# Performance work log

Measured on AMD Instinct MI355X. Metric: run time of the kernel, lower is better.

The kernel has to match this reference:

```python
import jax, jax.numpy as jnp
import numpy as np

N_NODES = 50000
N_EDGES = 800000


def gcn_layer(x, edge_index, W, b):
    # GCNConv with normalize=False: out[i] = sum_{(j->i) in E} (x_j @ W) + b
    src, dst = edge_index[0], edge_index[1]
    h = x @ W                          # [N, F_out] transform first (cheaper)
    msg = h[src]                       # [E, F_out] gather
    agg = jax.ops.segment_sum(msg, dst, num_segments=x.shape[0])  # scatter-sum
    return agg + b


def setup_inputs() -> dict:
    key = jax.random.key(0)
    ks = jax.random.split(key, 6)
    x = jax.random.normal(ks[0], (N_NODES, 128), dtype=jnp.float32)
    edge_index = jax.random.randint(ks[1], (2, N_EDGES), 0, N_NODES, dtype=jnp.int64)
    # Glorot-ish scaling for stability through 3 layers
    W1 = jax.random.normal(ks[2], (128, 256), dtype=jnp.float32) * (1.0 / np.sqrt(128))
    W2 = jax.random.normal(ks[3], (256, 256), dtype=jnp.float32) * (1.0 / np.sqrt(256))
    W3 = jax.random.normal(ks[4], (256, 256), dtype=jnp.float32) * (1.0 / np.sqrt(256))
    b1 = jnp.zeros((256,), jnp.float32)
    b2 = jnp.zeros((256,), jnp.float32)
    b3 = jnp.zeros((256,), jnp.float32)
    return {"x": x, "edge_index": edge_index, "W1": W1, "b1": b1,
            "W2": W2, "b2": b2, "W3": W3, "b3": b3}


def reference(x, edge_index, W1, b1, W2, b2, W3, b3):
    h = jax.nn.relu(gcn_layer(x, edge_index, W1, b1))
    h = jax.nn.relu(gcn_layer(h, edge_index, W2, b2))
    h = jax.nn.relu(gcn_layer(h, edge_index, W3, b3))
    return h
```

## Files before the change

kernel.cpp:

```cpp
#include <hip/hip_runtime.h>
#include <hip/hip_bf16.h>


#define NBIN 98
#define BINSH 9
#define CAP 10240

typedef short bf16x8 __attribute__((ext_vector_type(8)));
typedef float f32x4 __attribute__((ext_vector_type(4)));
typedef unsigned u32x4 __attribute__((ext_vector_type(4)));

__device__ __forceinline__ short f2bf(float f) {
    __hip_bfloat16 b = __float2bfloat16(f);
    return *reinterpret_cast<short*>(&b);
}

__device__ __forceinline__ void acc8(float* a, u32x4 v) {
#pragma unroll
    for (int i = 0; i < 4; ++i) {
        union { unsigned u; float f; } lo, hi;
        lo.u = v[i] << 16;
        hi.u = v[i] & 0xFFFF0000u;
        a[2 * i]     += lo.f;
        a[2 * i + 1] += hi.f;
    }
}

__global__ void prep(const float* __restrict__ W1, const float* __restrict__ W2,
                     const float* __restrict__ W3, const float4* __restrict__ x,
                     short* __restrict__ Wt1, short* __restrict__ Wt2,
                     short* __restrict__ Wt3, short* __restrict__ xb,
                     int* __restrict__ gcursor, int* __restrict__ off,
                     int E, int N) {
    int idx = blockIdx.x * 256 + threadIdx.x;
    if (idx < 32768) {
        int n = idx >> 7, k = idx & 127;
        Wt1[idx] = f2bf(W1[k * 256 + n]);
    } else if (idx < 98304) {
        int i = idx - 32768, n = i >> 8, k = i & 255;
        Wt2[i] = f2bf(W2[k * 256 + n]);
    } else if (idx < 163840) {
        int i = idx - 98304, n = i >> 8, k = i & 255;
        Wt3[i] = f2bf(W3[k * 256 + n]);
    } else {
        int i = idx - 163840;
        if (i < 1600000) {
            float4 v = x[i];
            short tmp[4] = { f2bf(v.x), f2bf(v.y), f2bf(v.z), f2bf(v.w) };
            *reinterpret_cast<uint2*>(&xb[i * 4]) = *reinterpret_cast<uint2*>(tmp);
        } else {
            int z = i - 1600000;
            if (z < NBIN) gcursor[z] = 0;
            if (z == NBIN) off[N] = E;
        }
    }
}


__launch_bounds__(256)
__global__ void bin_fill(const int* __restrict__ ei, int* __restrict__ gcursor,
                         unsigned* __restrict__ staging, int E) {
    __shared__ int h[NBIN];
    __shared__ int lstart[NBIN];
    __shared__ int gbase[NBIN];
    __shared__ int cur[NBIN];
    __shared__ int scan[256];
    __shared__ unsigned sorted[4096];
    const int t = threadIdx.x;
    for (int i = t; i < NBIN; i += 256) h[i] = 0;
    __syncthreads();
    const int base = blockIdx.x * 4096;
    unsigned w[16];
    int bin[16];
#pragma unroll
    for (int i = 0; i < 16; ++i) {
        int e = base + i * 256 + t;
        if (e < E) {
            int s = ei[e], d = ei[E + e];
            w[i] = ((unsigned)d << 16) | (unsigned)s;
            bin[i] = d >> BINSH;
            atomicAdd(&h[bin[i]], 1);
        } else bin[i] = -1;
    }
    __syncthreads();
    int v = (t < NBIN) ? h[t] : 0;
    scan[t] = v;
    __syncthreads();
    for (int d = 1; d < 256; d <<= 1) {
        int a = (t >= d) ? scan[t - d] : 0;
        __syncthreads();
        scan[t] += a;
        __syncthreads();
    }
    if (t < NBIN) {
        int ex = scan[t] - v;
        lstart[t] = ex;
        cur[t] = ex;
        gbase[t] = v ? atomicAdd(&gcursor[t], v) : 0;
    }
    __syncthreads();
#pragma unroll
    for (int i = 0; i < 16; ++i)
        if (bin[i] >= 0) sorted[atomicAdd(&cur[bin[i]], 1)] = w[i];
    __syncthreads();
    const int nvalid = min(4096, E - base);
    for (int i = t; i < nvalid; i += 256) {
        unsigned u = sorted[i];
        int b = (u >> 16) >> BINSH;
        staging[(size_t)b * CAP + gbase[b] + (i - lstart[b])] = u;
    }
}

__launch_bounds__(256)
__global__ void bin_finalize(const unsigned* __restrict__ staging,
                             const int* __restrict__ cnt,
                             int* __restrict__ off, int* __restrict__ csr, int N) {
    __shared__ int red[256];
    __shared__ int nd_c[512];
    __shared__ int nd_pos[512];
    __shared__ int psum[256];
    const int b = blockIdx.x, t = threadIdx.x;
    const int n = cnt[b];
    const unsigned* reg = staging + (size_t)b * CAP;

    red[t] = (t < b) ? cnt[t] : 0;
    nd_c[t] = 0; nd_c[t + 256] = 0;
    __syncthreads();
    for (int d = 128; d > 0; d >>= 1) {
        if (t < d) red[t] += red[t + d];
        __syncthreads();
    }
    const int gbase = red[0];

    for (int p = t; p < n; p += 256)
        atomicAdd(&nd_c[(reg[p] >> 16) & 511u], 1);
    __syncthreads();
    int c0 = nd_c[2 * t], c1 = nd_c[2 * t + 1];
    psum[t] = c0 + c1;
    __syncthreads();
    for (int d = 1; d < 256; d <<= 1) {
        int a = (t >= d) ? psum[t - d] : 0;
        __syncthreads();
        psum[t] += a;
        __syncthreads();
    }
    int ebase = gbase + (t ? psum[t - 1] : 0);
    int nb0 = b << BINSH;
    nd_pos[2 * t]     = ebase;
    nd_pos[2 * t + 1] = ebase + c0;
    if (nb0 + 2 * t < N)     off[nb0 + 2 * t]     = ebase;
    if (nb0 + 2 * t + 1 < N) off[nb0 + 2 * t + 1] = ebase + c0;
    __syncthreads();
    for (int p = t; p < n; p += 256) {
        unsigned v = reg[p];
        int pos = atomicAdd(&nd_pos[(v >> 16) & 511u], 1);
        csr[pos] = (int)(v & 0xFFFFu);
    }
}


__global__ void gather256(const short* __restrict__ h, short* __restrict__ agg,
                          const int* __restrict__ off, const int* __restrict__ csr,
                          int N) {
    const int gw = (blockIdx.x * blockDim.x + threadIdx.x) >> 6;
    if (gw >= N) return;
    const int lane = threadIdx.x & 63;
    const int half = lane >> 5, l = lane & 31;
    const int col = l * 8;
    const int base = off[gw];
    const int d = off[gw + 1] - base;

    float acc[8];
#pragma unroll
    for (int q = 0; q < 8; ++q) acc[q] = 0.0f;

    int j = 0;
    for (; j + 8 <= d; j += 8) {
        int s0 = csr[base + j + half];
        int s1 = csr[base + j + 2 + half];
        int s2 = csr[base + j + 4 + half];
        int s3 = csr[base + j + 6 + half];
        u32x4 v0 = *reinterpret_cast<const u32x4*>(h + (size_t)s0 * 256 + col);
        u32x4 v1 = *reinterpret_cast<const u32x4*>(h + (size_t)s1 * 256 + col);
        u32x4 v2 = *reinterpret_cast<const u32x4*>(h + (size_t)s2 * 256 + col);
        u32x4 v3 = *reinterpret_cast<const u32x4*>(h + (size_t)s3 * 256 + col);
        acc8(acc, v0); acc8(acc, v1); acc8(acc, v2); acc8(acc, v3);
    }
    for (; j + 2 <= d; j += 2) {
        int s = csr[base + j + half];
        u32x4 v = *reinterpret_cast<const u32x4*>(h + (size_t)s * 256 + col);
        acc8(acc, v);
    }
    if (j < d && half == 0) {
        int s = csr[base + j];
        u32x4 v = *reinterpret_cast<const u32x4*>(h + (size_t)s * 256 + col);
        acc8(acc, v);
    }
#pragma unroll
    for (int q = 0; q < 8; ++q) acc[q] += __shfl_xor(acc[q], 32);
    if (half == 0) {
        short o[8];
#pragma unroll
        for (int q = 0; q < 8; ++q) o[q] = f2bf(acc[q]);
        __builtin_nontemporal_store(*reinterpret_cast<u32x4*>(o),
            reinterpret_cast<u32x4*>(agg + (size_t)gw * 256 + col));
    }
}

__global__ void gather128(const short* __restrict__ h, short* __restrict__ agg,
                          const int* __restrict__ off, const int* __restrict__ csr,
                          int N) {
    const int gw = (blockIdx.x * blockDim.x + threadIdx.x) >> 6;
    if (gw >= N) return;
    const int lane = threadIdx.x & 63;
    const int q4 = lane >> 4, l = lane & 15;
    const int col = l * 8;
    const int base = off[gw];
    const int d = off[gw + 1] - base;

    float acc[8];
#pragma unroll
    for (int q = 0; q < 8; ++q) acc[q] = 0.0f;

    int j = 0;
    for (; j + 8 <= d; j += 8) {
        int s0 = csr[base + j + q4];
        int s1 = csr[base + j + 4 + q4];
        u32x4 v0 = *reinterpret_cast<const u32x4*>(h + (size_t)s0 * 128 + col);
        u32x4 v1 = *reinterpret_cast<const u32x4*>(h + (size_t)s1 * 128 + col);
        acc8(acc, v0); acc8(acc, v1);
    }
    for (; j + 4 <= d; j += 4) {
        int s = csr[base + j + q4];
        u32x4 v = *reinterpret_cast<const u32x4*>(h + (size_t)s * 128 + col);
        acc8(acc, v);
    }
    int rem = d - j;
    if (q4 < rem) {
        int s = csr[base + j + q4];
        u32x4 v = *reinterpret_cast<const u32x4*>(h + (size_t)s * 128 + col);
        acc8(acc, v);
    }
#pragma unroll
    for (int q = 0; q < 8; ++q) {
        acc[q] += __shfl_xor(acc[q], 32);
        acc[q] += __shfl_xor(acc[q], 16);
    }
    if (q4 == 0) {
        short o[8];
#pragma unroll
        for (int q = 0; q < 8; ++q) o[q] = f2bf(acc[q]);
        __builtin_nontemporal_store(*reinterpret_cast<u32x4*>(o),
            reinterpret_cast<u32x4*>(agg + (size_t)gw * 128 + col));
    }
}


template <typename OutT>
__launch_bounds__(512)
__global__ void gemm_bias_relu(const short* __restrict__ A, const short* __restrict__ Wt,
                               const float* __restrict__ bias, OutT* __restrict__ out,
                               int M, int K) {
    __shared__ short As[128][72];
    __shared__ short Bs[256][72];

    const int tid = threadIdx.x;
    const int lane = tid & 63, wid = tid >> 6;
    const int wr = wid >> 2, wc = wid & 3;
    const int lr = lane & 15, lg = lane >> 4;
    const int m0 = blockIdx.x * 128;

    f32x4 acc[4][4];
#pragma unroll
    for (int i = 0; i < 4; ++i)
#pragma unroll
        for (int j = 0; j < 4; ++j)
#pragma unroll
            for (int r = 0; r < 4; ++r) acc[i][j][r] = 0.0f;

    const int srA = tid >> 2;
    const int scA = (tid & 3) << 4;
    const int srB = tid >> 1;
    const int scB = (tid & 1) << 5;

    for (int k0 = 0; k0 < K; k0 += 64) {
        __syncthreads();
        {
            int gm = m0 + srA;
            if (gm < M) {
                const uint4* ap = reinterpret_cast<const uint4*>(A + (size_t)gm * K + k0 + scA);
                *reinterpret_cast<uint4*>(&As[srA][scA])     = ap[0];
                *reinterpret_cast<uint4*>(&As[srA][scA + 8]) = ap[1];
            } else {
                uint4 z = {0, 0, 0, 0};
                *reinterpret_cast<uint4*>(&As[srA][scA])     = z;
                *reinterpret_cast<uint4*>(&As[srA][scA + 8]) = z;
            }
            const uint4* bp = reinterpret_cast<const uint4*>(Wt + (size_t)srB * K + k0 + scB);
            *reinterpret_cast<uint4*>(&Bs[srB][scB])      = bp[0];
            *reinterpret_cast<uint4*>(&Bs[srB][scB + 8])  = bp[1];
            *reinterpret_cast<uint4*>(&Bs[srB][scB + 16]) = bp[2];
            *reinterpret_cast<uint4*>(&Bs[srB][scB + 24]) = bp[3];
        }
        __syncthreads();

#pragma unroll
        for (int ksub = 0; ksub < 2; ++ksub) {
            const int kb = ksub * 32 + 4 * lg;
            bf16x8 a[4], b[4];
#pragma unroll
            for (int mi = 0; mi < 4; ++mi) {
                int row = wr * 64 + mi * 16 + lr;
                uint2* pa = reinterpret_cast<uint2*>(&a[mi]);
                pa[0] = *reinterpret_cast<const uint2*>(&As[row][kb]);
                pa[1] = *reinterpret_cast<const uint2*>(&As[row][kb + 16]);
            }
#pragma unroll
            for (int ni = 0; ni < 4; ++ni) {
                int row = wc * 64 + ni * 16 + lr;
                uint2* pb = reinterpret_cast<uint2*>(&b[ni]);
                pb[0] = *reinterpret_cast<const uint2*>(&Bs[row][kb]);
                pb[1] = *reinterpret_cast<const uint2*>(&Bs[row][kb + 16]);
            }
#pragma unroll
            for (int mi = 0; mi < 4; ++mi)
#pragma unroll
                for (int ni = 0; ni < 4; ++ni)
                    acc[mi][ni] = __builtin_amdgcn_mfma_f32_16x16x32_bf16(a[mi], b[ni], acc[mi][ni], 0, 0, 0);
        }
    }

    float bv[4];
#pragma unroll
    for (int ni = 0; ni < 4; ++ni) bv[ni] = bias[wc * 64 + ni * 16 + lr];
#pragma unroll
    for (int mi = 0; mi < 4; ++mi) {
        int gmBase = m0 + wr * 64 + mi * 16 + 4 * lg;
#pragma unroll
        for (int r = 0; r < 4; ++r) {
            int gm = gmBase + r;
            if (gm >= M) continue;
#pragma unroll
            for (int ni = 0; ni < 4; ++ni) {
                int gn = wc * 64 + ni * 16 + lr;
                float v = acc[mi][ni][r] + bv[ni];
                v = v > 0.0f ? v : 0.0f;
                if constexpr (sizeof(OutT) == 2)
                    __builtin_nontemporal_store((OutT)f2bf(v), &out[(size_t)gm * 256 + gn]);
                else
                    __builtin_nontemporal_store((OutT)v, &out[(size_t)gm * 256 + gn]);
            }
        }
    }
}

extern "C" void kernel_launch(void* const* d_in, const int* in_sizes, int n_in,
                              void* d_out, int out_size, void* d_ws, size_t ws_size,
                              hipStream_t stream) {
    const float* x  = (const float*)d_in[0];
    const int*   ei = (const int*)d_in[1];
    const float* W1 = (const float*)d_in[2];
    const float* b1 = (const float*)d_in[3];
    const float* W2 = (const float*)d_in[4];
    const float* b2 = (const float*)d_in[5];
    const float* W3 = (const float*)d_in[6];
    const float* b3 = (const float*)d_in[7];
    float* out = (float*)d_out;
    short* hb  = (short*)d_out;

    const int Nn = 50000, E = 800000, F0 = 128, F = 256;
    const int EB = (E + 4095) / 4096;

    short* aggb = (short*)d_ws;
    short* xb   = aggb + (size_t)Nn * F;
    short* Wt1  = xb + (size_t)Nn * F0;
    short* Wt2  = Wt1 + F0 * F;
    short* Wt3  = Wt2 + F * F;
    int* off     = (int*)(Wt3 + F * F);
    int* gcursor = off + Nn + 1;
    unsigned* staging = (unsigned*)(gcursor + NBIN);
    int* csr     = (int*)(staging + (size_t)NBIN * CAP);

    prep<<<(163840 + 1600000 + NBIN + 1 + 255) / 256, 256, 0, stream>>>(
        W1, W2, W3, (const float4*)x, Wt1, Wt2, Wt3, xb, gcursor, off, E, Nn);

    bin_fill<<<EB, 256, 0, stream>>>(ei, gcursor, staging, E);
    bin_finalize<<<NBIN, 256, 0, stream>>>(staging, gcursor, off, csr, Nn);

    const int gemmGrid = (Nn + 127) / 128;
    const int gatherBlocks = (Nn * 64 + 255) / 256;

    gather128<<<gatherBlocks, 256, 0, stream>>>(xb, aggb, off, csr, Nn);
    gemm_bias_relu<short><<<gemmGrid, 512, 0, stream>>>(aggb, Wt1, b1, hb, Nn, F0);

    gather256<<<gatherBlocks, 256, 0, stream>>>(hb, aggb, off, csr, Nn);
    gemm_bias_relu<short><<<gemmGrid, 512, 0, stream>>>(aggb, Wt2, b2, hb, Nn, F);

    gather256<<<gatherBlocks, 256, 0, stream>>>(hb, aggb, off, csr, Nn);
    gemm_bias_relu<float><<<gemmGrid, 512, 0, stream>>>(aggb, Wt3, b3, out, Nn, F);
}
```

Measured before the change: 241.8 us.

## Fuse neighbor gather into GEMM per layer, staging aggregated rows in LDS

Each layer's gather and GEMM now run as one kernel. Every block gathers 64 destination rows directly into shared memory, then multiplies them by the transposed weights with MFMA, applying bias and ReLU. This removes the global write and re-read of the aggregated buffer and halves the kernel launches. The cost is a smaller M tile (64 rows), so weight tiles are reloaded more often per row, and a serial gather phase inside each block that the GEMM cannot overlap. The workspace is also re-laid out, with separate h1/h2 buffers and staging aliased onto h2.

```diff
diff --git a/kernel.cpp b/kernel.cpp
--- a/kernel.cpp
+++ b/kernel.cpp
@@ -159,143 +159,124 @@
 }
 
 
-__global__ void gather256(const short* __restrict__ h, short* __restrict__ agg,
-                          const int* __restrict__ off, const int* __restrict__ csr,
-                          int N) {
-    const int gw = (blockIdx.x * blockDim.x + threadIdx.x) >> 6;
-    if (gw >= N) return;
-    const int lane = threadIdx.x & 63;
-    const int half = lane >> 5, l = lane & 31;
-    const int col = l * 8;
-    const int base = off[gw];
-    const int d = off[gw + 1] - base;
-
-    float acc[8];
-#pragma unroll
-    for (int q = 0; q < 8; ++q) acc[q] = 0.0f;
-
-    int j = 0;
-    for (; j + 8 <= d; j += 8) {
-        int s0 = csr[base + j + half];
-        int s1 = csr[base + j + 2 + half];
-        int s2 = csr[base + j + 4 + half];
-        int s3 = csr[base + j + 6 + half];
-        u32x4 v0 = *reinterpret_cast<const u32x4*>(h + (size_t)s0 * 256 + col);
-        u32x4 v1 = *reinterpret_cast<const u32x4*>(h + (size_t)s1 * 256 + col);
-        u32x4 v2 = *reinterpret_cast<const u32x4*>(h + (size_t)s2 * 256 + col);
-        u32x4 v3 = *reinterpret_cast<const u32x4*>(h + (size_t)s3 * 256 + col);
-        acc8(acc, v0); acc8(acc, v1); acc8(acc, v2); acc8(acc, v3);
-    }
-    for (; j + 2 <= d; j += 2) {
-        int s = csr[base + j + half];
-        u32x4 v = *reinterpret_cast<const u32x4*>(h + (size_t)s * 256 + col);
-        acc8(acc, v);
-    }
-    if (j < d && half == 0) {
-        int s = csr[base + j];
-        u32x4 v = *reinterpret_cast<const u32x4*>(h + (size_t)s * 256 + col);
-        acc8(acc, v);
-    }
-#pragma unroll
-    for (int q = 0; q < 8; ++q) acc[q] += __shfl_xor(acc[q], 32);
-    if (half == 0) {
-        short o[8];
-#pragma unroll
-        for (int q = 0; q < 8; ++q) o[q] = f2bf(acc[q]);
-        __builtin_nontemporal_store(*reinterpret_cast<u32x4*>(o),
-            reinterpret_cast<u32x4*>(agg + (size_t)gw * 256 + col));
-    }
-}
-
-__global__ void gather128(const short* __restrict__ h, short* __restrict__ agg,
-                          const int* __restrict__ off, const int* __restrict__ csr,
-                          int N) {
-    const int gw = (blockIdx.x * blockDim.x + threadIdx.x) >> 6;
-    if (gw >= N) return;
-    const int lane = threadIdx.x & 63;
-    const int q4 = lane >> 4, l = lane & 15;
-    const int col = l * 8;
-    const int base = off[gw];
-    const int d = off[gw + 1] - base;
-
-    float acc[8];
-#pragma unroll
-    for (int q = 0; q < 8; ++q) acc[q] = 0.0f;
-
-    int j = 0;
-    for (; j + 8 <= d; j += 8) {
-        int s0 = csr[base + j + q4];
-        int s1 = csr[base + j + 4 + q4];
-        u32x4 v0 = *reinterpret_cast<const u32x4*>(h + (size_t)s0 * 128 + col);
-        u32x4 v1 = *reinterpret_cast<const u32x4*>(h + (size_t)s1 * 128 + col);
-        acc8(acc, v0); acc8(acc, v1);
-    }
-    for (; j + 4 <= d; j += 4) {
-        int s = csr[base + j + q4];
-        u32x4 v = *reinterpret_cast<const u32x4*>(h + (size_t)s * 128 + col);
-        acc8(acc, v);
-    }
-    int rem = d - j;
-    if (q4 < rem) {
-        int s = csr[base + j + q4];
-        u32x4 v = *reinterpret_cast<const u32x4*>(h + (size_t)s * 128 + col);
-        acc8(acc, v);
-    }
-#pragma unroll
-    for (int q = 0; q < 8; ++q) {
-        acc[q] += __shfl_xor(acc[q], 32);
-        acc[q] += __shfl_xor(acc[q], 16);
-    }
-    if (q4 == 0) {
-        short o[8];
-#pragma unroll
-        for (int q = 0; q < 8; ++q) o[q] = f2bf(acc[q]);
-        __builtin_nontemporal_store(*reinterpret_cast<u32x4*>(o),
-            reinterpret_cast<u32x4*>(agg + (size_t)gw * 128 + col));
-    }
-}
-
-
-template <typename OutT>
-__launch_bounds__(512)
-__global__ void gemm_bias_relu(const short* __restrict__ A, const short* __restrict__ Wt,
-                               const float* __restrict__ bias, OutT* __restrict__ out,
-                               int M, int K) {
-    __shared__ short As[128][72];
+template <int K, typename OutT>
+__launch_bounds__(512, 4)
+__global__ void fused_layer(const short* __restrict__ h,
+                            const short* __restrict__ Wt,
+                            const float* __restrict__ bias,
+                            OutT* __restrict__ out,
+                            const int* __restrict__ off,
+                            const int* __restrict__ csr, int N) {
+    __shared__ short As[64][K + 8];
     __shared__ short Bs[256][72];
 
     const int tid = threadIdx.x;
     const int lane = tid & 63, wid = tid >> 6;
+    const int m0 = blockIdx.x * 64;
+
+    if constexpr (K == 256) {
+        const int half = lane >> 5, l = lane & 31;
+        const int col = l * 8;
+        for (int r8 = 0; r8 < 8; ++r8) {
+            const int row = wid * 8 + r8;
+            const int gw = m0 + row;
+            int base = 0, d = 0;
+            if (gw < N) { base = off[gw]; d = off[gw + 1] - base; }
+            float acc[8];
+#pragma unroll
+            for (int q = 0; q < 8; ++q) acc[q] = 0.0f;
+            int j = 0;
+            for (; j + 8 <= d; j += 8) {
+                int s0 = csr[base + j + half];
+                int s1 = csr[base + j + 2 + half];
+                int s2 = csr[base + j + 4 + half];
+                int s3 = csr[base + j + 6 + half];
+                u32x4 v0 = *reinterpret_cast<const u32x4*>(h + (size_t)s0 * 256 + col);
+                u32x4 v1 = *reinterpret_cast<const u32x4*>(h + (size_t)s1 * 256 + col);
+                u32x4 v2 = *reinterpret_cast<const u32x4*>(h + (size_t)s2 * 256 + col);
+                u32x4 v3 = *reinterpret_cast<const u32x4*>(h + (size_t)s3 * 256 + col);
+                acc8(acc, v0); acc8(acc, v1); acc8(acc, v2); acc8(acc, v3);
+            }
+            for (; j + 2 <= d; j += 2) {
+                int s = csr[base + j + half];
+                u32x4 v = *reinterpret_cast<const u32x4*>(h + (size_t)s * 256 + col);
+                acc8(acc, v);
+            }
+            if (j < d && half == 0) {
+                int s = csr[base + j];
+                u32x4 v = *reinterpret_cast<const u32x4*>(h + (size_t)s * 256 + col);
+                acc8(acc, v);
+            }
+#pragma unroll
+            for (int q = 0; q < 8; ++q) acc[q] += __shfl_xor(acc[q], 32);
+            if (half == 0) {
+                short o[8];
+#pragma unroll
+                for (int q = 0; q < 8; ++q) o[q] = f2bf(acc[q]);
+                *reinterpret_cast<u32x4*>(&As[row][col]) = *reinterpret_cast<u32x4*>(o);
+            }
+        }
+    } else {
+        const int q4 = lane >> 4, l = lane & 15;
+        const int col = l * 8;
+        for (int r8 = 0; r8 < 8; ++r8) {
+            const int row = wid * 8 + r8;
+            const int gw = m0 + row;
+            int base = 0, d = 0;
+            if (gw < N) { base = off[gw]; d = off[gw + 1] - base; }
+            float acc[8];
+#pragma unroll
+            for (int q = 0; q < 8; ++q) acc[q] = 0.0f;
+            int j = 0;
+            for (; j + 8 <= d; j += 8) {
+                int s0 = csr[base + j + q4];
+                int s1 = csr[base + j + 4 + q4];
+                u32x4 v0 = *reinterpret_cast<const u32x4*>(h + (size_t)s0 * 128 + col);
+                u32x4 v1 = *reinterpret_cast<const u32x4*>(h + (size_t)s1 * 128 + col);
+                acc8(acc, v0); acc8(acc, v1);
+            }
+            for (; j + 4 <= d; j += 4) {
+                int s = csr[base + j + q4];
+                u32x4 v = *reinterpret_cast<const u32x4*>(h + (size_t)s * 128 + col);
+                acc8(acc, v);
+            }
+            int rem = d - j;
+            if (q4 < rem) {
+                int s = csr[base + j + q4];
+                u32x4 v = *reinterpret_cast<const u32x4*>(h + (size_t)s * 128 + col);
+                acc8(acc, v);
+            }
+#pragma unroll
+            for (int q = 0; q < 8; ++q) {
+                acc[q] += __shfl_xor(acc[q], 32);
+                acc[q] += __shfl_xor(acc[q], 16);
+            }
+            if (q4 == 0) {
+                short o[8];
+#pragma unroll
+                for (int q = 0; q < 8; ++q) o[q] = f2bf(acc[q]);
+                *reinterpret_cast<u32x4*>(&As[row][col]) = *reinterpret_cast<u32x4*>(o);
+            }
+        }
+    }
+
     const int wr = wid >> 2, wc = wid & 3;
     const int lr = lane & 15, lg = lane >> 4;
-    const int m0 = blockIdx.x * 128;
-
-    f32x4 acc[4][4];
-#pragma unroll
-    for (int i = 0; i < 4; ++i)
+
+    f32x4 acc[2][4];
+#pragma unroll
+    for (int i = 0; i < 2; ++i)
 #pragma unroll
         for (int j = 0; j < 4; ++j)
 #pragma unroll
             for (int r = 0; r < 4; ++r) acc[i][j][r] = 0.0f;
 
-    const int srA = tid >> 2;
-    const int scA = (tid & 3) << 4;
     const int srB = tid >> 1;
     const int scB = (tid & 1) << 5;
 
     for (int k0 = 0; k0 < K; k0 += 64) {
         __syncthreads();
         {
-            int gm = m0 + srA;
-            if (gm < M) {
-                const uint4* ap = reinterpret_cast<const uint4*>(A + (size_t)gm * K + k0 + scA);
-                *reinterpret_cast<uint4*>(&As[srA][scA])     = ap[0];
-                *reinterpret_cast<uint4*>(&As[srA][scA + 8]) = ap[1];
-            } else {
-                uint4 z = {0, 0, 0, 0};
-                *reinterpret_cast<uint4*>(&As[srA][scA])     = z;
-                *reinterpret_cast<uint4*>(&As[srA][scA + 8]) = z;
-            }
             const uint4* bp = reinterpret_cast<const uint4*>(Wt + (size_t)srB * K + k0 + scB);
             *reinterpret_cast<uint4*>(&Bs[srB][scB])      = bp[0];
             *reinterpret_cast<uint4*>(&Bs[srB][scB + 8])  = bp[1];
@@ -307,13 +288,13 @@
 #pragma unroll
         for (int ksub = 0; ksub < 2; ++ksub) {
             const int kb = ksub * 32 + 4 * lg;
-            bf16x8 a[4], b[4];
-#pragma unroll
-            for (int mi = 0; mi < 4; ++mi) {
-                int row = wr * 64 + mi * 16 + lr;
+            bf16x8 a[2], b[4];
+#pragma unroll
+            for (int mi = 0; mi < 2; ++mi) {
+                int row = wr * 32 + mi * 16 + lr;
                 uint2* pa = reinterpret_cast<uint2*>(&a[mi]);
-                pa[0] = *reinterpret_cast<const uint2*>(&As[row][kb]);
-                pa[1] = *reinterpret_cast<const uint2*>(&As[row][kb + 16]);
+                pa[0] = *reinterpret_cast<const uint2*>(&As[row][k0 + kb]);
+                pa[1] = *reinterpret_cast<const uint2*>(&As[row][k0 + kb + 16]);
             }
 #pragma unroll
             for (int ni = 0; ni < 4; ++ni) {
@@ -323,7 +304,7 @@
                 pb[1] = *reinterpret_cast<const uint2*>(&Bs[row][kb + 16]);
             }
 #pragma unroll
-            for (int mi = 0; mi < 4; ++mi)
+            for (int mi = 0; mi < 2; ++mi)
 #pragma unroll
                 for (int ni = 0; ni < 4; ++ni)
                     acc[mi][ni] = __builtin_amdgcn_mfma_f32_16x16x32_bf16(a[mi], b[ni], acc[mi][ni], 0, 0, 0);
@@ -334,12 +315,12 @@
 #pragma unroll
     for (int ni = 0; ni < 4; ++ni) bv[ni] = bias[wc * 64 + ni * 16 + lr];
 #pragma unroll
-    for (int mi = 0; mi < 4; ++mi) {
-        int gmBase = m0 + wr * 64 + mi * 16 + 4 * lg;
+    for (int mi = 0; mi < 2; ++mi) {
+        int gmBase = m0 + wr * 32 + mi * 16 + 4 * lg;
 #pragma unroll
         for (int r = 0; r < 4; ++r) {
             int gm = gmBase + r;
-            if (gm >= M) continue;
+            if (gm >= N) continue;
 #pragma unroll
             for (int ni = 0; ni < 4; ++ni) {
                 int gn = wc * 64 + ni * 16 + lr;
@@ -366,20 +347,20 @@
     const float* W3 = (const float*)d_in[6];
     const float* b3 = (const float*)d_in[7];
     float* out = (float*)d_out;
-    short* hb  = (short*)d_out;
 
     const int Nn = 50000, E = 800000, F0 = 128, F = 256;
     const int EB = (E + 4095) / 4096;
 
-    short* aggb = (short*)d_ws;
-    short* xb   = aggb + (size_t)Nn * F;
-    short* Wt1  = xb + (size_t)Nn * F0;
-    short* Wt2  = Wt1 + F0 * F;
-    short* Wt3  = Wt2 + F * F;
+    short* h1 = (short*)d_ws;
+    short* h2 = h1 + (size_t)Nn * F;
+    short* xb = h2;
+    unsigned* staging = (unsigned*)(h2 + (size_t)Nn * F0);
+    short* Wt1 = h2 + (size_t)Nn * F;
+    short* Wt2 = Wt1 + F0 * F;
+    short* Wt3 = Wt2 + F * F;
     int* off     = (int*)(Wt3 + F * F);
     int* gcursor = off + Nn + 1;
-    unsigned* staging = (unsigned*)(gcursor + NBIN);
-    int* csr     = (int*)(staging + (size_t)NBIN * CAP);
+    int* csr     = gcursor + NBIN;
 
     prep<<<(163840 + 1600000 + NBIN + 1 + 255) / 256, 256, 0, stream>>>(
         W1, W2, W3, (const float4*)x, Wt1, Wt2, Wt3, xb, gcursor, off, E, Nn);
@@ -387,15 +368,9 @@
     bin_fill<<<EB, 256, 0, stream>>>(ei, gcursor, staging, E);
     bin_finalize<<<NBIN, 256, 0, stream>>>(staging, gcursor, off, csr, Nn);
 
-    const int gemmGrid = (Nn + 127) / 128;
-    const int gatherBlocks = (Nn * 64 + 255) / 256;
-
-    gather128<<<gatherBlocks, 256, 0, stream>>>(xb, aggb, off, csr, Nn);
-    gemm_bias_relu<short><<<gemmGrid, 512, 0, stream>>>(aggb, Wt1, b1, hb, Nn, F0);
-
-    gather256<<<gatherBlocks, 256, 0, stream>>>(hb, aggb, off, csr, Nn);
-    gemm_bias_relu<short><<<gemmGrid, 512, 0, stream>>>(aggb, Wt2, b2, hb, Nn, F);
-
-    gather256<<<gatherBlocks, 256, 0, stream>>>(hb, aggb, off, csr, Nn);
-    gemm_bias_relu<float><<<gemmGrid, 512, 0, stream>>>(aggb, Wt3, b3, out, Nn, F);
-}
+    const int fusedGrid = (Nn + 63) / 64;
+
+    fused_layer<128, short><<<fusedGrid, 512, 0, stream>>>(xb, Wt1, b1, h1, off, csr, Nn);
+    fused_layer<256, short><<<fusedGrid, 512, 0, stream>>>(h1, Wt2, b2, h2, off, csr, Nn);
+    fused_layer<256, float><<<fusedGrid, 512, 0, stream>>>(h2, Wt3, b3, out, off, csr, Nn);
+}
```

New measurement: 271.3 us. 12.2% more time.
